# Performance work log

Measured on AMD Instinct MI355X. Metric: run time of the kernel, lower is better.

The kernel has to match this reference:

```python
import jax, jax.numpy as jnp
import numpy as np

B, Q, DIM, HEADS, HEAD_DIM, KV = 32, 4, 2048, 16, 128, 8192


def setup_inputs() -> dict:
    key = jax.random.key(0)
    ks = jax.random.split(key, 9)
    s = 0.02
    return {
        'x': jax.random.normal(ks[0], (B, Q, DIM), jnp.float32),
        'attn_bias': jax.random.normal(ks[1], (B, HEADS, Q, KV), jnp.float32),
        'cache_k': jax.random.normal(ks[2], (B, KV, HEAD_DIM), jnp.float32),
        'cache_v': jax.random.normal(ks[3], (B, KV, HEAD_DIM), jnp.float32),
        'wq': jax.random.normal(ks[4], (DIM, HEADS, HEAD_DIM), jnp.float32) * s,
        'bq': jnp.zeros((HEADS, HEAD_DIM), jnp.float32),
        'wk': jax.random.normal(ks[5], (DIM, HEAD_DIM), jnp.float32) * s,
        'bk': jnp.zeros((HEAD_DIM,), jnp.float32),
        'wv': jax.random.normal(ks[6], (DIM, HEAD_DIM), jnp.float32) * s,
        'bv': jnp.zeros((HEAD_DIM,), jnp.float32),
        'wo': jax.random.normal(ks[7], (HEADS, HEAD_DIM, DIM), jnp.float32) * s,
        'bo': jnp.zeros((DIM,), jnp.float32),
    }


def reference(x, attn_bias, cache_k, cache_v, wq, bq, wk, bk, wv, bv, wo, bo):
    q_len = x.shape[1]
    # projections (MQA: shared single-head K/V)
    q = jnp.einsum('bqd,dhe->bqhe', x, wq) + bq          # [B,Q,H,hd]
    k_new = x @ wk + bk                                   # [B,Q,hd]
    v_new = x @ wv + bv
    # rolling KV cache update: shift left by q_len, write new tokens at end
    k = jnp.roll(cache_k, -q_len, axis=1).at[:, -q_len:].set(k_new)  # [B,KV,hd]
    v = jnp.roll(cache_v, -q_len, axis=1).at[:, -q_len:].set(v_new)
    scale = 1.0 / (k.shape[-1] ** 0.5)
    p = jnp.einsum('bqhe,bke->bhqk', q, k) * scale        # [B,H,Q,KV]
    a = jax.nn.softmax(p + attn_bias, axis=-1)
    o = jnp.einsum('bhqk,bke->bqhe', a, v)                # [B,Q,H,hd]
    return jnp.einsum('bqhe,hed->bqd', o, wo) + bo        # [B,Q,DIM]
```

## Files before the change

kernel.cpp:

```cpp
#include <hip/hip_runtime.h>
#include <cstddef>
#include <cstdint>

#define BATCH 32
#define QL 4
#define DIM 2048
#define NH 16
#define HD 128
#define KVLEN 8192
#define HQ 64
#define CHUNK 512
#define NCK 16
#define KT 64
#define NT 8

typedef __attribute__((ext_vector_type(8))) short bf16x8;
typedef __attribute__((ext_vector_type(4))) float f32x4;

__device__ __forceinline__ unsigned short cvt_bf16(float f) {
    unsigned int u = __builtin_bit_cast(unsigned int, f);
    u += 0x7fffu + ((u >> 16) & 1u);
    return (unsigned short)(u >> 16);
}
__device__ __forceinline__ unsigned int pack2(float a, float b) {
    return (unsigned int)cvt_bf16(a) | ((unsigned int)cvt_bf16(b) << 16);
}
__device__ __forceinline__ float bf16_to_f32(unsigned short s) {
    unsigned int u = ((unsigned int)s) << 16;
    return __builtin_bit_cast(float, u);
}
__device__ __forceinline__ bf16x8 mk_frag(unsigned int a, unsigned int b,
                                          unsigned int c, unsigned int d) {
    unsigned int t[4] = {a, b, c, d};
    return *(const bf16x8*)t;
}

template<int VARIANT>
__global__ __launch_bounds__(256) void gemm_kernel(
    const float* __restrict__ A,
    const float* __restrict__ w0p, const float* __restrict__ w1p,
    const float* __restrict__ w2p,
    const float* __restrict__ b0p, const float* __restrict__ b1p,
    const float* __restrict__ b2p,
    float* __restrict__ o0, float* __restrict__ o1, float* __restrict__ o2)
{
    const int n0 = blockIdx.x * 64;
    const int m0 = blockIdx.y * 64;
    const int kz = blockIdx.z * 512;
    const int tid = threadIdx.x;
    const int wave = tid >> 6, lane = tid & 63;
    const int l15 = lane & 15, quad = lane >> 4;

    const float* W; const float* Bv; int ldw, nc;
    if (VARIANT == 0) {
        if (n0 >= 2176)      { W = w2p; Bv = b2p; ldw = 128;  nc = n0 - 2176; }
        else if (n0 >= 2048) { W = w1p; Bv = b1p; ldw = 128;  nc = n0 - 2048; }
        else                 { W = w0p; Bv = b0p; ldw = 2048; nc = n0; }
    } else { W = w0p; Bv = b0p; ldw = 2048; nc = n0; }

    __shared__ alignas(16) unsigned short a_s[64][72];
    __shared__ alignas(16) unsigned short w_s[64][68];

    const int wn = tid & 63;
    const int wk0 = (tid >> 6) * 4;

    f32x4 acc[4];
    #pragma unroll
    for (int nt = 0; nt < 4; ++nt) acc[nt] = (f32x4){0.f, 0.f, 0.f, 0.f};

    float4 apre[4];
    float wpre[4][4];

    #pragma unroll
    for (int ii = 0; ii < 4; ++ii) {
        int f = tid + 256 * ii, r = f >> 4, c4 = (f & 15) << 2;
        apre[ii] = *(const float4*)&A[(size_t)(m0 + r) * DIM + kz + c4];
    }
    #pragma unroll
    for (int sub = 0; sub < 4; ++sub) {
        int k0 = kz + wk0 + 16 * sub;
        const float* wp = W + (size_t)k0 * ldw + nc + wn;
        #pragma unroll
        for (int j = 0; j < 4; ++j) wpre[sub][j] = wp[(size_t)j * ldw];
    }

    for (int it = 0; it < 8; ++it) {
        __syncthreads();
        #pragma unroll
        for (int ii = 0; ii < 4; ++ii) {
            int f = tid + 256 * ii, r = f >> 4, c4 = (f & 15) << 2;
            *(uint2*)&a_s[r][c4] =
                make_uint2(pack2(apre[ii].x, apre[ii].y), pack2(apre[ii].z, apre[ii].w));
        }
        #pragma unroll
        for (int sub = 0; sub < 4; ++sub) {
            int k0 = wk0 + 16 * sub;
            *(uint2*)&w_s[wn][k0] =
                make_uint2(pack2(wpre[sub][0], wpre[sub][1]),
                           pack2(wpre[sub][2], wpre[sub][3]));
        }
        __syncthreads();
        if (it + 1 < 8) {
            const int kb = kz + (it + 1) * 64;
            #pragma unroll
            for (int ii = 0; ii < 4; ++ii) {
                int f = tid + 256 * ii, r = f >> 4, c4 = (f & 15) << 2;
                apre[ii] = *(const float4*)&A[(size_t)(m0 + r) * DIM + kb + c4];
            }
            #pragma unroll
            for (int sub = 0; sub < 4; ++sub) {
                int k0 = kb + wk0 + 16 * sub;
                const float* wp = W + (size_t)k0 * ldw + nc + wn;
                #pragma unroll
                for (int j = 0; j < 4; ++j) wpre[sub][j] = wp[(size_t)j * ldw];
            }
        }
        #pragma unroll
        for (int kf = 0; kf < 2; ++kf) {
            bf16x8 af = *(const bf16x8*)&a_s[16 * wave + l15][kf * 32 + quad * 8];
            #pragma unroll
            for (int nt = 0; nt < 4; ++nt) {
                uint2 lo = *(const uint2*)&w_s[nt * 16 + l15][kf * 32 + quad * 8];
                uint2 hi = *(const uint2*)&w_s[nt * 16 + l15][kf * 32 + quad * 8 + 4];
                bf16x8 wf = mk_frag(lo.x, lo.y, hi.x, hi.y);
                acc[nt] = __builtin_amdgcn_mfma_f32_16x16x32_bf16(af, wf, acc[nt], 0, 0, 0);
            }
        }
    }
    const bool addb = (blockIdx.z == 0);
    #pragma unroll
    for (int nt = 0; nt < 4; ++nt)
        #pragma unroll
        for (int reg = 0; reg < 4; ++reg) {
            int row = m0 + 16 * wave + quad * 4 + reg;
            int col = n0 + nt * 16 + l15;
            float s = acc[nt][reg];
            if (VARIANT == 1) {
                atomicAdd(&o0[(size_t)row * DIM + col], s + (addb ? Bv[col] : 0.f));
            } else {
                int b = row >> 2, q = row & 3;
                if (col < 2048) {
                    int h = col >> 7, e = col & 127;
                    atomicAdd(&o0[((size_t)(b * 64 + h * 4 + q)) * 128 + e],
                              s + (addb ? b0p[col] : 0.f));
                } else if (col < 2176) {
                    int e = col - 2048;
                    atomicAdd(&o1[(size_t)row * 128 + e], s + (addb ? b1p[e] : 0.f));
                } else {
                    int e = col - 2176;
                    atomicAdd(&o2[(size_t)row * 128 + e], s + (addb ? b2p[e] : 0.f));
                }
            }
        }
}


#define PREFETCH_KV(tb_, kp_, vp_)                                            \
    do {                                                                      \
        _Pragma("unroll")                                                     \
        for (int i = 0; i < 8; ++i) {                                         \
            int f = tid + 256 * i;                                            \
            int row = f >> 5, e0 = (f & 31) << 2;                             \
            int kv = (tb_) + row;                                             \
            const float* pk = (kv < KVLEN - QL)                               \
                ? cachek + ((size_t)b * KVLEN + kv + QL) * HD + e0            \
                : kws + ((size_t)b * QL + (kv - (KVLEN - QL))) * HD + e0;     \
            kp_[i] = *(const float4*)pk;                                      \
        }                                                                     \
        _Pragma("unroll")                                                     \
        for (int i = 0; i < 8; ++i) {                                         \
            int kv0 = (tb_) + (vkq + 2 * i) * 4;                              \
            _Pragma("unroll")                                                 \
            for (int j = 0; j < 4; ++j) {                                     \
                int kv = kv0 + j;                                             \
                const float* pv = (kv < KVLEN - QL)                           \
                    ? cachev + ((size_t)b * KVLEN + kv + QL) * HD + ve        \
                    : vws + ((size_t)b * QL + (kv - (KVLEN - QL))) * HD + ve; \
                vp_[i][j] = *pv;                                              \
            }                                                                 \
        }                                                                     \
    } while (0)

#define PREFETCH_B(toff_)                                                     \
    do {                                                                      \
        _Pragma("unroll")                                                     \
        for (int nt = 0; nt < 4; ++nt)                                        \
            _Pragma("unroll")                                                 \
            for (int reg = 0; reg < 4; ++reg)                                 \
                bpre[nt * 4 + reg] = bptr[reg][(toff_) + nt * 16];            \
    } while (0)

#define STORE_LDS(kp_, vp_)                                                   \
    do {                                                                      \
        _Pragma("unroll")                                                     \
        for (int i = 0; i < 8; ++i) {                                         \
            int f = tid + 256 * i;                                            \
            int row = f >> 5, e0 = (f & 31) << 2;                             \
            *(uint2*)&k_s[row][e0] =                                          \
                make_uint2(pack2(kp_[i].x, kp_[i].y),                         \
                           pack2(kp_[i].z, kp_[i].w));                        \
        }                                                                     \
        _Pragma("unroll")                                                     \
        for (int i = 0; i < 8; ++i) {                                         \
            int kv0 = (vkq + 2 * i) * 4;                                      \
            *(uint2*)&v_sT[ve][kv0] =                                         \
                make_uint2(pack2(vp_[i][0], vp_[i][1]),                       \
                           pack2(vp_[i][2], vp_[i][3]));                      \
        }                                                                     \
    } while (0)

#define COMPUTE_TILE(bias_)                                                   \
    do {                                                                      \
        f32x4 sacc[4];                                                        \
        _Pragma("unroll")                                                     \
        for (int nt = 0; nt < 4; ++nt) sacc[nt] = (f32x4){0.f, 0.f, 0.f, 0.f};\
        __builtin_amdgcn_s_setprio(1);                                        \
        _Pragma("unroll")                                                     \
        for (int kf = 0; kf < 4; ++kf) {                                      \
            _Pragma("unroll")                                                 \
            for (int nt = 0; nt < 4; ++nt) {                                  \
                bf16x8 kfb = *(const bf16x8*)&k_s[nt * 16 + l15][kf * 32 + quad * 8]; \
                sacc[nt] = __builtin_amdgcn_mfma_f32_16x16x32_bf16(qf[kf], kfb, sacc[nt], 0, 0, 0); \
            }                                                                 \
        }                                                                     \
        __builtin_amdgcn_s_setprio(0);                                        \
        _Pragma("unroll")                                                     \
        for (int nt = 0; nt < 4; ++nt)                                        \
            _Pragma("unroll")                                                 \
            for (int reg = 0; reg < 4; ++reg) {                               \
                float s = sacc[nt][reg] * scale + bias_[nt * 4 + reg];        \
                float p = __expf(s);                                          \
                unsigned short pb = cvt_bf16(p);                              \
                lrow[reg] += bf16_to_f32(pb);                                 \
                p_s[wave][quad * 4 + reg][nt * 16 + l15] = pb;                \
            }                                                                 \
        __builtin_amdgcn_s_setprio(1);                                        \
        _Pragma("unroll")                                                     \
        for (int kfp = 0; kfp < 2; ++kfp) {                                   \
            uint2 plo = *(const uint2*)&p_s[wave][l15][kfp * 32 + quad * 8];  \
            uint2 phi = *(const uint2*)&p_s[wave][l15][kfp * 32 + quad * 8 + 4]; \
            bf16x8 pf = mk_frag(plo.x, plo.y, phi.x, phi.y);                  \
            _Pragma("unroll")                                                 \
            for (int n8 = 0; n8 < 8; ++n8) {                                  \
                uint2 vlo = *(const uint2*)&v_sT[n8 * 16 + l15][kfp * 32 + quad * 8]; \
                uint2 vhi = *(const uint2*)&v_sT[n8 * 16 + l15][kfp * 32 + quad * 8 + 4]; \
                bf16x8 vf = mk_frag(vlo.x, vlo.y, vhi.x, vhi.y);              \
                oa[n8] = __builtin_amdgcn_mfma_f32_16x16x32_bf16(pf, vf, oa[n8], 0, 0, 0); \
            }                                                                 \
        }                                                                     \
        __builtin_amdgcn_s_setprio(0);                                        \
    } while (0)

__global__ __launch_bounds__(256, 2) void attn_kernel(
    const float* __restrict__ qws, const float* __restrict__ kws,
    const float* __restrict__ vws,
    const float* __restrict__ cachek, const float* __restrict__ cachev,
    const float* __restrict__ abias,
    float* __restrict__ opart, float* __restrict__ lpart)
{
    const int ck = blockIdx.x;
    const int b  = blockIdx.y;
    const int tid = threadIdx.x;
    const int wave = tid >> 6, lane = tid & 63;
    const int l15 = lane & 15, quad = lane >> 4;
    const float scale = 0.08838834764831845f;

    __shared__ alignas(16) unsigned short k_s[KT][136];
    __shared__ alignas(16) unsigned short v_sT[HD][68];
    __shared__ alignas(16) unsigned short p_s[4][16][72];

    bf16x8 qf[4];
    {
        const float* qrow = qws + ((size_t)b * HQ + 16 * wave + l15) * HD;
        #pragma unroll
        for (int kf = 0; kf < 4; ++kf) {
            float4 f0 = *(const float4*)&qrow[kf * 32 + quad * 8];
            float4 f1 = *(const float4*)&qrow[kf * 32 + quad * 8 + 4];
            qf[kf] = mk_frag(pack2(f0.x, f0.y), pack2(f0.z, f0.w),
                             pack2(f1.x, f1.y), pack2(f1.z, f1.w));
        }
    }

    const int kbase0 = ck * CHUNK;
    const int ve = tid & 127;
    const int vkq = (tid >> 7);

    const float* bptr[4];
    #pragma unroll
    for (int reg = 0; reg < 4; ++reg) {
        int hq = 16 * wave + quad * 4 + reg;
        int h = hq >> 2, q = hq & 3;
        bptr[reg] = abias + (((size_t)(b * NH + h)) * QL + q) * KVLEN + kbase0 + l15;
    }

    float4 kpre0[8], kpre1[8];
    float vpre0[8][4], vpre1[8][4];
    float bpre[16];

    PREFETCH_KV(kbase0, kpre0, vpre0);
    PREFETCH_KV(kbase0 + KT, kpre1, vpre1);
    PREFETCH_B(0);

    f32x4 oa[8];
    #pragma unroll
    for (int n8 = 0; n8 < 8; ++n8) oa[n8] = (f32x4){0.f, 0.f, 0.f, 0.f};
    float lrow[4] = {0.f, 0.f, 0.f, 0.f};

    for (int tt = 0; tt < NT; tt += 2) {
        {
            __syncthreads();
            STORE_LDS(kpre0, vpre0);
            float bias[16];
            #pragma unroll
            for (int j = 0; j < 16; ++j) bias[j] = bpre[j];
            __syncthreads();
            if (tt + 2 < NT) PREFETCH_KV(kbase0 + (tt + 2) * KT, kpre0, vpre0);
            PREFETCH_B((tt + 1) * KT);
            COMPUTE_TILE(bias);
        }
        {
            __syncthreads();
            STORE_LDS(kpre1, vpre1);
            float bias[16];
            #pragma unroll
            for (int j = 0; j < 16; ++j) bias[j] = bpre[j];
            __syncthreads();
            if (tt + 3 < NT) PREFETCH_KV(kbase0 + (tt + 3) * KT, kpre1, vpre1);
            if (tt + 2 < NT) PREFETCH_B((tt + 2) * KT);
            COMPUTE_TILE(bias);
        }
    }
    #pragma unroll
    for (int reg = 0; reg < 4; ++reg) {
        float v = lrow[reg];
        v += __shfl_xor(v, 1);
        v += __shfl_xor(v, 2);
        v += __shfl_xor(v, 4);
        v += __shfl_xor(v, 8);
        lrow[reg] = v;
    }
    const size_t obase = ((size_t)(b * NCK + ck)) * HQ * HD;
    #pragma unroll
    for (int n8 = 0; n8 < 8; ++n8)
        #pragma unroll
        for (int reg = 0; reg < 4; ++reg) {
            int hq = 16 * wave + quad * 4 + reg;
            int e = n8 * 16 + l15;
            opart[obase + (size_t)hq * HD + e] = oa[n8][reg];
        }
    if (l15 == 0) {
        #pragma unroll
        for (int reg = 0; reg < 4; ++reg) {
            int hq = 16 * wave + quad * 4 + reg;
            lpart[(size_t)(b * NCK + ck) * HQ + hq] = lrow[reg];
        }
    }
}

__global__ __launch_bounds__(128) void combine_kernel(
    const float* __restrict__ opart, const float* __restrict__ lpart,
    float* __restrict__ ored, float* __restrict__ outz)
{
    const int bh = blockIdx.x;
    const int b = bh >> 6, hq = bh & 63;
    const int e = threadIdx.x;
    outz[(size_t)bh * 128 + e] = 0.f;
    float lt = 0.f, ov = 0.f;
    #pragma unroll
    for (int c = 0; c < NCK; ++c) {
        lt += lpart[(b * NCK + c) * HQ + hq];
        ov += opart[((size_t)(b * NCK + c) * HQ + hq) * HD + e];
    }
    int h = hq >> 2, q = hq & 3;
    ored[(size_t)(b * QL + q) * DIM + h * HD + e] = ov / lt;
}

extern "C" void kernel_launch(void* const* d_in, const int* in_sizes, int n_in,
                              void* d_out, int out_size, void* d_ws, size_t ws_size,
                              hipStream_t stream)
{
    const float* x   = (const float*)d_in[0];
    const float* ab  = (const float*)d_in[1];
    const float* cK  = (const float*)d_in[2];
    const float* cV  = (const float*)d_in[3];
    const float* wq  = (const float*)d_in[4];
    const float* bq  = (const float*)d_in[5];
    const float* wk  = (const float*)d_in[6];
    const float* bk  = (const float*)d_in[7];
    const float* wv  = (const float*)d_in[8];
    const float* bv  = (const float*)d_in[9];
    const float* wo  = (const float*)d_in[10];
    const float* bo  = (const float*)d_in[11];
    float* out = (float*)d_out;

    float* ws   = (float*)d_ws;
    float* wsq  = ws;
    float* wsk  = wsq + 262144;
    float* wsv  = wsk + 16384;
    float* wsop = wsv + 16384;
    float* wsl  = wsop + 4194304;
    float* wsor = wsl + 32768;

    hipMemsetAsync(ws, 0, (size_t)(262144 + 16384 + 16384) * sizeof(float),
                   stream);

    gemm_kernel<0><<<dim3(36, 2, 4), 256, 0, stream>>>(
        x, wq, wk, wv, bq, bk, bv, wsq, wsk, wsv);
    attn_kernel<<<dim3(NCK, BATCH), 256, 0, stream>>>(
        wsq, wsk, wsv, cK, cV, ab, wsop, wsl);
    combine_kernel<<<BATCH * HQ, 128, 0, stream>>>(wsop, wsl, wsor, out);
    gemm_kernel<1><<<dim3(32, 2, 4), 256, 0, stream>>>(
        wsor, wo, nullptr, nullptr, bo, nullptr, nullptr, out, nullptr, nullptr);
}
```

Baseline: 435.3 us.

## Move KV double buffering from registers into LDS with one barrier per tile

K/V tiles are now double-buffered in shared memory (k_s0/k_s1, v_s0/v_s1) rather than in two sets of prefetch registers. Each tile is written to the idle LDS buffer right after the current tile's compute, and the next global prefetch is issued at that point. This drops one __syncthreads per tile and halves the prefetch register footprint, aiming to cut barrier stalls and register pressure under launch_bounds(256,2). In exchange, LDS use roughly doubles, which could limit occupancy, and global loads have less time in flight before they are consumed.

```diff
diff --git a/kernel.cpp b/kernel.cpp
--- a/kernel.cpp
+++ b/kernel.cpp
@@ -155,7 +155,7 @@
 }
 
 
-#define PREFETCH_KV(tb_, kp_, vp_)                                            \
+#define PREFETCH_KV(tb_)                                                      \
     do {                                                                      \
         _Pragma("unroll")                                                     \
         for (int i = 0; i < 8; ++i) {                                         \
@@ -165,7 +165,7 @@
             const float* pk = (kv < KVLEN - QL)                               \
                 ? cachek + ((size_t)b * KVLEN + kv + QL) * HD + e0            \
                 : kws + ((size_t)b * QL + (kv - (KVLEN - QL))) * HD + e0;     \
-            kp_[i] = *(const float4*)pk;                                      \
+            kpre[i] = *(const float4*)pk;                                     \
         }                                                                     \
         _Pragma("unroll")                                                     \
         for (int i = 0; i < 8; ++i) {                                         \
@@ -176,7 +176,7 @@
                 const float* pv = (kv < KVLEN - QL)                           \
                     ? cachev + ((size_t)b * KVLEN + kv + QL) * HD + ve        \
                     : vws + ((size_t)b * QL + (kv - (KVLEN - QL))) * HD + ve; \
-                vp_[i][j] = *pv;                                              \
+                vpre[i][j] = *pv;                                             \
             }                                                                 \
         }                                                                     \
     } while (0)
@@ -190,26 +190,26 @@
                 bpre[nt * 4 + reg] = bptr[reg][(toff_) + nt * 16];            \
     } while (0)
 
-#define STORE_LDS(kp_, vp_)                                                   \
+#define STORE_LDS(ks_, vs_)                                                   \
     do {                                                                      \
         _Pragma("unroll")                                                     \
         for (int i = 0; i < 8; ++i) {                                         \
             int f = tid + 256 * i;                                            \
             int row = f >> 5, e0 = (f & 31) << 2;                             \
-            *(uint2*)&k_s[row][e0] =                                          \
-                make_uint2(pack2(kp_[i].x, kp_[i].y),                         \
-                           pack2(kp_[i].z, kp_[i].w));                        \
+            *(uint2*)&ks_[row][e0] =                                          \
+                make_uint2(pack2(kpre[i].x, kpre[i].y),                       \
+                           pack2(kpre[i].z, kpre[i].w));                      \
         }                                                                     \
         _Pragma("unroll")                                                     \
         for (int i = 0; i < 8; ++i) {                                         \
             int kv0 = (vkq + 2 * i) * 4;                                      \
-            *(uint2*)&v_sT[ve][kv0] =                                         \
-                make_uint2(pack2(vp_[i][0], vp_[i][1]),                       \
-                           pack2(vp_[i][2], vp_[i][3]));                      \
+            *(uint2*)&vs_[ve][kv0] =                                          \
+                make_uint2(pack2(vpre[i][0], vpre[i][1]),                     \
+                           pack2(vpre[i][2], vpre[i][3]));                    \
         }                                                                     \
     } while (0)
 
-#define COMPUTE_TILE(bias_)                                                   \
+#define COMPUTE_TILE(bias_, ks_, vs_)                                         \
     do {                                                                      \
         f32x4 sacc[4];                                                        \
         _Pragma("unroll")                                                     \
@@ -219,7 +219,7 @@
         for (int kf = 0; kf < 4; ++kf) {                                      \
             _Pragma("unroll")                                                 \
             for (int nt = 0; nt < 4; ++nt) {                                  \
-                bf16x8 kfb = *(const bf16x8*)&k_s[nt * 16 + l15][kf * 32 + quad * 8]; \
+                bf16x8 kfb = *(const bf16x8*)&ks_[nt * 16 + l15][kf * 32 + quad * 8]; \
                 sacc[nt] = __builtin_amdgcn_mfma_f32_16x16x32_bf16(qf[kf], kfb, sacc[nt], 0, 0, 0); \
             }                                                                 \
         }                                                                     \
@@ -242,8 +242,8 @@
             bf16x8 pf = mk_frag(plo.x, plo.y, phi.x, phi.y);                  \
             _Pragma("unroll")                                                 \
             for (int n8 = 0; n8 < 8; ++n8) {                                  \
-                uint2 vlo = *(const uint2*)&v_sT[n8 * 16 + l15][kfp * 32 + quad * 8]; \
-                uint2 vhi = *(const uint2*)&v_sT[n8 * 16 + l15][kfp * 32 + quad * 8 + 4]; \
+                uint2 vlo = *(const uint2*)&vs_[n8 * 16 + l15][kfp * 32 + quad * 8]; \
+                uint2 vhi = *(const uint2*)&vs_[n8 * 16 + l15][kfp * 32 + quad * 8 + 4]; \
                 bf16x8 vf = mk_frag(vlo.x, vlo.y, vhi.x, vhi.y);              \
                 oa[n8] = __builtin_amdgcn_mfma_f32_16x16x32_bf16(pf, vf, oa[n8], 0, 0, 0); \
             }                                                                 \
@@ -265,8 +265,10 @@
     const int l15 = lane & 15, quad = lane >> 4;
     const float scale = 0.08838834764831845f;
 
-    __shared__ alignas(16) unsigned short k_s[KT][136];
-    __shared__ alignas(16) unsigned short v_sT[HD][68];
+    __shared__ alignas(16) unsigned short k_s0[KT][136];
+    __shared__ alignas(16) unsigned short k_s1[KT][136];
+    __shared__ alignas(16) unsigned short v_s0[HD][68];
+    __shared__ alignas(16) unsigned short v_s1[HD][68];
     __shared__ alignas(16) unsigned short p_s[4][16][72];
 
     bf16x8 qf[4];
@@ -293,12 +295,13 @@
         bptr[reg] = abias + (((size_t)(b * NH + h)) * QL + q) * KVLEN + kbase0 + l15;
     }
 
-    float4 kpre0[8], kpre1[8];
-    float vpre0[8][4], vpre1[8][4];
+    float4 kpre[8];
+    float vpre[8][4];
     float bpre[16];
 
-    PREFETCH_KV(kbase0, kpre0, vpre0);
-    PREFETCH_KV(kbase0 + KT, kpre1, vpre1);
+    PREFETCH_KV(kbase0);
+    STORE_LDS(k_s0, v_s0);
+    PREFETCH_KV(kbase0 + KT);
     PREFETCH_B(0);
 
     f32x4 oa[8];
@@ -309,25 +312,25 @@
     for (int tt = 0; tt < NT; tt += 2) {
         {
             __syncthreads();
-            STORE_LDS(kpre0, vpre0);
             float bias[16];
             #pragma unroll
             for (int j = 0; j < 16; ++j) bias[j] = bpre[j];
-            __syncthreads();
-            if (tt + 2 < NT) PREFETCH_KV(kbase0 + (tt + 2) * KT, kpre0, vpre0);
             PREFETCH_B((tt + 1) * KT);
-            COMPUTE_TILE(bias);
+            COMPUTE_TILE(bias, k_s0, v_s0);
+            STORE_LDS(k_s1, v_s1);
+            if (tt + 2 < NT) PREFETCH_KV(kbase0 + (tt + 2) * KT);
         }
         {
             __syncthreads();
-            STORE_LDS(kpre1, vpre1);
             float bias[16];
             #pragma unroll
             for (int j = 0; j < 16; ++j) bias[j] = bpre[j];
-            __syncthreads();
-            if (tt + 3 < NT) PREFETCH_KV(kbase0 + (tt + 3) * KT, kpre1, vpre1);
             if (tt + 2 < NT) PREFETCH_B((tt + 2) * KT);
-            COMPUTE_TILE(bias);
+            COMPUTE_TILE(bias, k_s1, v_s1);
+            if (tt + 2 < NT) {
+                STORE_LDS(k_s0, v_s0);
+                if (tt + 3 < NT) PREFETCH_KV(kbase0 + (tt + 3) * KT);
+            }
         }
     }
     #pragma unroll
```

Result: faster. 398.6 us (-8.4%).
